# Optimization experiments

Measured on AMD Instinct MI355X. Metric: run time of the kernel, lower is better.

The kernel has to match this reference:

```python
import jax, jax.numpy as jnp
import numpy as np

NUM_HEADS = 8
WINDOW = 33  # must be odd for seq length to be preserved


def setup_inputs() -> dict:
    key = jax.random.key(0)
    ks = jax.random.split(key, 7)
    B, S, E = 4, 2048, 256
    sc = 1.0 / np.sqrt(E)
    return {
        "x": jax.random.normal(ks[0], (B, S, E), dtype=jnp.float32),
        "Wq": jax.random.normal(ks[1], (E, E), dtype=jnp.float32) * sc,
        "bq": jax.random.normal(ks[2], (E,), dtype=jnp.float32) * 0.01,
        "Wk": jax.random.normal(ks[3], (E, E), dtype=jnp.float32) * sc,
        "bk": jax.random.normal(ks[4], (E,), dtype=jnp.float32) * 0.01,
        "Wv": jax.random.normal(ks[5], (E, E), dtype=jnp.float32) * sc,
        "bv": jax.random.normal(ks[6], (E,), dtype=jnp.float32) * 0.01,
    }


def reference(x, Wq, bq, Wk, bk, Wv, bv):
    B, S, E = x.shape
    H = NUM_HEADS
    D = E // H
    W = WINDOW
    pad = (W - 1) // 2
    scale = D ** (-0.5)

    def heads(t):  # [B,S,E] -> [B,H,S,D]
        return t.reshape(B, S, H, D).transpose(0, 2, 1, 3)

    q = heads(x @ Wq + bq)
    k = heads(x @ Wk + bk)
    v = heads(x @ Wv + bv)

    K = S - W + 1  # number of k/v windows (unfold with step=1)
    kv_idx = jnp.arange(K)[:, None] + jnp.arange(W)[None, :]  # [K,W]
    k_unf = k[:, :, kv_idx, :]  # [B,H,K,W,D]
    v_unf = v[:, :, kv_idx, :]  # [B,H,K,W,D]

    q_pad = jnp.pad(q, ((0, 0), (0, 0), (pad, pad), (0, 0)))  # zero pad seq
    q_idx = jnp.arange(S)[:, None] + jnp.arange(W)[None, :]  # [S,W]
    q_unf = q_pad[:, :, q_idx, :]  # [B,H,S,W,D]

    # contract over BOTH window and head dim (faithful to the torch einsums)
    scores = jnp.einsum('bhqwd,bhkwd->bhqk', q_unf, k_unf) * scale  # [B,H,S,K]
    attn = jax.nn.softmax(scores, axis=-1)
    out = jnp.einsum('bhqk,bhkwd->bhqd', attn, v_unf)  # sums v over window too
    return out.transpose(0, 2, 1, 3).reshape(B, S, E)
```

## Files before the change

kernel.cpp:

```cpp
#include <hip/hip_runtime.h>
#include <hip/hip_bf16.h>
#include <math.h>

#define BB   4
#define SS   2048
#define EE   256
#define HH   8
#define DD   32
#define WW   33
#define KKN  (SS - WW + 1)
#define SCALE 0.17677669529663687f
#define FMAX 20.0f
#define SCALE2 0.25503486f
#define FM2    28.853900817779268f

typedef __attribute__((ext_vector_type(8))) short short8v;
typedef __attribute__((ext_vector_type(4))) short short4v;
typedef __attribute__((ext_vector_type(4))) float float4v;

__device__ __forceinline__ short f2bf(float f) {
    union { __hip_bfloat16 h; short s; } c;
    c.h = __float2bfloat16(f);
    return c.s;
}

#if __has_builtin(__builtin_amdgcn_exp2f)
__device__ __forceinline__ float exp2_fast(float x) { return __builtin_amdgcn_exp2f(x); }
#else
__device__ __forceinline__ float exp2_fast(float x) { return __expf(x * 0.6931471805599453f); }
#endif

__global__ __launch_bounds__(256) void qkv_kernel(
    const float* __restrict__ x,
    const float* __restrict__ Wq, const float* __restrict__ bq,
    const float* __restrict__ Wk, const float* __restrict__ bk,
    const float* __restrict__ Wv, const float* __restrict__ bv,
    short* __restrict__ qo, short* __restrict__ ko, float* __restrict__ vo)
{
    __shared__ alignas(16) float xs[64][68];
    __shared__ alignas(16) float ws[64][68];

    const int t   = threadIdx.x;
    const int r0  = blockIdx.x * 64;
    const int ct  = blockIdx.y;
    const int mat = ct >> 2;
    const int cm0 = (ct & 3) * 64;
    const float* Wm   = (mat == 0) ? Wq : (mat == 1) ? Wk : Wv;
    const float* bias = (mat == 0) ? bq : (mat == 1) ? bk : bv;

    const int tr = t >> 4, tc = t & 15;

    float acc[4][4];
#pragma unroll
    for (int i = 0; i < 4; i++)
#pragma unroll
        for (int j = 0; j < 4; j++) acc[i][j] = 0.f;

    for (int ec = 0; ec < 4; ec++) {
        const int e0 = ec * 64;
        __syncthreads();
#pragma unroll
        for (int i = 0; i < 4; i++) {
            int L = t + i * 256;
            int r = L >> 4, c4 = (L & 15) * 4;
            *(float4*)&xs[r][c4] = *(const float4*)(x  + (size_t)(r0 + r) * EE + e0 + c4);
            *(float4*)&ws[r][c4] = *(const float4*)(Wm + (size_t)(e0 + r) * EE + cm0 + c4);
        }
        __syncthreads();

#pragma unroll
        for (int eg = 0; eg < 16; eg++) {
            float4 xv[4], wv4[4];
#pragma unroll
            for (int i = 0; i < 4; i++) xv[i]  = *(const float4*)&xs[tr * 4 + i][eg * 4];
#pragma unroll
            for (int j = 0; j < 4; j++) wv4[j] = *(const float4*)&ws[eg * 4 + j][tc * 4];
            const float* w0p = (const float*)&wv4[0];
            const float* w1p = (const float*)&wv4[1];
            const float* w2p = (const float*)&wv4[2];
            const float* w3p = (const float*)&wv4[3];
#pragma unroll
            for (int i = 0; i < 4; i++)
#pragma unroll
                for (int j = 0; j < 4; j++)
                    acc[i][j] = acc[i][j] + xv[i].x * w0p[j] + xv[i].y * w1p[j]
                                          + xv[i].z * w2p[j] + xv[i].w * w3p[j];
        }
    }

    const int cmb = cm0 + tc * 4;
    const int h = cmb >> 5, d0 = cmb & 31;
    float b4[4];
#pragma unroll
    for (int j = 0; j < 4; j++) b4[j] = bias[cmb + j];

#pragma unroll
    for (int i = 0; i < 4; i++) {
        int row = r0 + tr * 4 + i;
        int b_  = row >> 11;
        int s   = row & 2047;
        size_t o = (((size_t)(b_ * HH + h)) * SS + s) * DD + d0;
        if (mat == 2) {
            float4 vv;
            vv.x = acc[i][0] + b4[0]; vv.y = acc[i][1] + b4[1];
            vv.z = acc[i][2] + b4[2]; vv.w = acc[i][3] + b4[3];
            *(float4*)(vo + o) = vv;
        } else {
            short4v sv;
            sv.x = f2bf(acc[i][0] + b4[0]); sv.y = f2bf(acc[i][1] + b4[1]);
            sv.z = f2bf(acc[i][2] + b4[2]); sv.w = f2bf(acc[i][3] + b4[3]);
            *(short4v*)(((mat == 0) ? qo : ko) + o) = sv;
        }
    }
}

__global__ __launch_bounds__(256) void vs_kernel(
    const float* __restrict__ v, short* __restrict__ vsT)
{
    const int t   = threadIdx.x;
    const int d4  = t & 7;
    const int kkb = blockIdx.x * 32 + (t >> 3);
    const int bh  = blockIdx.y;
    if (kkb >= 252) return;
    const int kb0 = kkb * 8;

    const float4* vp = (const float4*)(v + ((size_t)bh * SS + kb0) * DD) + d4;
    float4 rbuf[7];
    float4 acc = {0.f, 0.f, 0.f, 0.f};
#pragma unroll
    for (int w = 0; w < WW; w++) {
        float4 xv = vp[w * 8];
        if (w < 7) rbuf[w] = xv;
        acc.x += xv.x; acc.y += xv.y; acc.z += xv.z; acc.w += xv.w;
    }
    short8v sh[4];
    sh[0][0] = f2bf(acc.x); sh[1][0] = f2bf(acc.y);
    sh[2][0] = f2bf(acc.z); sh[3][0] = f2bf(acc.w);
#pragma unroll
    for (int s = 1; s < 8; s++) {
        float4 sub = rbuf[s - 1];
        float4 add = vp[(s + 32) * 8];
        acc.x += add.x - sub.x; acc.y += add.y - sub.y;
        acc.z += add.z - sub.z; acc.w += add.w - sub.w;
        sh[0][s] = f2bf(acc.x); sh[1][s] = f2bf(acc.y);
        sh[2][s] = f2bf(acc.z); sh[3][s] = f2bf(acc.w);
    }
#pragma unroll
    for (int j = 0; j < 4; j++) {
        short* op = vsT + ((size_t)bh * DD + 4 * d4 + j) * KKN + kb0;
        *(short8v*)op = sh[j];
    }
}

__global__ __launch_bounds__(256, 4) void attn_kernel(
    const short* __restrict__ qg, const short* __restrict__ kg,
    const short* __restrict__ vsTg, float* __restrict__ out)
{
    __shared__ alignas(16) short QbS[64][40];
    __shared__ alignas(16) short Kb[128][40];
    __shared__ alignas(16) short Gst[96][72];
    __shared__ alignas(16) short vT[2][32][72];
    __shared__ float lrow[32];

    short (*Qb)[40] = QbS;
    short (*pb)[72] = (short (*)[72])QbS;

    const int t  = threadIdx.x;
    const int qt = blockIdx.x;
    const int bh = blockIdx.y;
    const int q0 = qt * 32;

    const short* qb   = qg   + (size_t)bh * SS * DD;
    const short* kb   = kg   + (size_t)bh * SS * DD;
    const short* vsTb = vsTg + (size_t)bh * DD * KKN;

    const int lane = t & 63, wv = t >> 6;
    const int quad = lane >> 4, lr = lane & 15;
    const int ptm = wv >> 1, ptn = wv & 1;
    const int jcol = 64 + (t & 7);

    {
        short8v z = {0, 0, 0, 0, 0, 0, 0, 0};
        short* g = &Gst[0][0];
        for (int i = t; i < 864; i += 256) *(short8v*)(g + 8 * i) = z;
    }

    {
        int row = t >> 2, c8 = (t & 3) * 8;
        int gq = q0 - 16 + row;
        if (gq >= 0 && gq < SS) {
            *(short8v*)&Qb[row][c8] = *(const short8v*)(qb + (size_t)gq * DD + c8);
        } else {
            float4 z = {0.f, 0.f, 0.f, 0.f};
            *(float4*)&Qb[row][c8] = z;
        }
        *(short8v*)&Kb[row][c8]      = *(const short8v*)(kb + (size_t)row * DD + c8);
        *(short8v*)&Kb[64 + row][c8] = *(const short8v*)(kb + (size_t)(64 + row) * DD + c8);
    }
    if (t < 32) lrow[t] = 0.f;
    __syncthreads();

    short8v Qf[4];
#pragma unroll
    for (int tq = 0; tq < 4; tq++)
        Qf[tq] = *(const short8v*)&Qb[tq * 16 + lr][quad * 8];

    short8v Uf[2][2];
#pragma unroll
    for (int qit = 0; qit < 2; qit++)
#pragma unroll
        for (int ch = 0; ch < 2; ch++) {
            short8v u;
#pragma unroll
            for (int j = 0; j < 8; j++) {
                int m  = ch * 32 + quad * 8 + j;
                int qi = qit * 16 + lr;
                u[j] = (qi <= m && m <= qi + 32) ? (short)0x3F80 : (short)0;
            }
            Uf[qit][ch] = u;
        }

    float4v acc = {0.f, 0.f, 0.f, 0.f};
    float lsum[2] = {0.f, 0.f};
    const int npass = (wv < 2) ? 2 : 1;

    for (int kt = 0; kt < 32; kt++) {
        const int k0 = kt * 64;
        {
            int d_ = t >> 3, c8 = (t & 7) * 8;
            int col = k0 + c8; if (col > KKN - 8) col = KKN - 8;
            *(short8v*)&vT[kt & 1][d_][c8] =
                *(const short8v*)(vsTb + (size_t)d_ * KKN + col);
        }

        for (int pass = 0; pass < npass; pass++) {
            const int tk = wv + pass * 4;
            const int gr = k0 + tk * 16 + lr;
            const short8v A = *(const short8v*)&Kb[gr & 127][quad * 8];
#pragma unroll
            for (int tq = 0; tq < 4; tq++) {
                const int del = tk - tq;
                if (del < -2 || del > 4) continue;
                float4v c0 = {0.f, 0.f, 0.f, 0.f};
                c0 = __builtin_amdgcn_mfma_f32_16x16x32_bf16(A, Qf[tq], c0, 0, 0, 0);
                const int i   = tq * 16 + lr;
                const int j2b = tk * 16 + quad * 4 - i + 31;
                short* gbase = &Gst[0][i];
#pragma unroll
                for (int e = 0; e < 4; e++) {
                    int j2 = j2b + e;
                    short* dst = ((unsigned)j2 < 95u) ? (gbase + j2 * 72)
                                                      : (gbase + 95 * 72);
                    *dst = f2bf(c0[e]);
                }
            }
        }

        if (kt > 0) {
            const short8v Ap0 = *(const short8v*)&pb[ptm * 16 + lr][quad * 8];
            const short8v Ap1 = *(const short8v*)&pb[ptm * 16 + lr][32 + quad * 8];
            const short8v Bv0 = *(const short8v*)&vT[(kt - 1) & 1][ptn * 16 + lr][quad * 8];
            const short8v Bv1 = *(const short8v*)&vT[(kt - 1) & 1][ptn * 16 + lr][32 + quad * 8];
            acc = __builtin_amdgcn_mfma_f32_16x16x32_bf16(Ap0, Bv0, acc, 0, 0, 0);
            acc = __builtin_amdgcn_mfma_f32_16x16x32_bf16(Ap1, Bv1, acc, 0, 0, 0);
        }
        __syncthreads();

        if (kt < 31) {
            int r2 = t >> 2, c8 = (t & 3) * 8;
            int g  = k0 + 128 + r2;
            int ga = (g < SS) ? g : (SS - 1);
            *(short8v*)&Kb[g & 127][c8] = *(const short8v*)(kb + (size_t)ga * DD + c8);
        }

        const unsigned lim = (kt == 31) ? 32u : 64u;
        if (kt == 31) {
            short4v z4 = {0, 0, 0, 0};
            int zr = t >> 3, zc = (t & 7) * 4 + 32;
            *(short4v*)&pb[zr][zc] = z4;
        }

        for (int pass = 0; pass < npass; pass++) {
            const int tile = wv + pass * 4;
            const int jrow = tile * 16 + lr;
            const short8v A0f = *(const short8v*)&Gst[jrow][quad * 8];
            const short8v A1f = *(const short8v*)&Gst[jrow][32 + quad * 8];
#pragma unroll
            for (int qit = 0; qit < 2; qit++) {
                float4v D = {0.f, 0.f, 0.f, 0.f};
                D = __builtin_amdgcn_mfma_f32_16x16x32_bf16(A0f, Uf[qit][0], D, 0, 0, 0);
                D = __builtin_amdgcn_mfma_f32_16x16x32_bf16(A1f, Uf[qit][1], D, 0, 0, 0);
                const int qi  = qit * 16 + lr;
                const int kib = qi + tile * 16 + quad * 4 - 31;
                short* prow = &pb[qi][0];
#pragma unroll
                for (int e = 0; e < 4; e++) {
                    int ki = kib + e;
                    float p = exp2_fast(fmaf(D[e], SCALE2, -FM2));
                    bool ok = (unsigned)ki < lim;
                    short* dst = ok ? (prow + ki) : (prow + jcol);
                    *dst = f2bf(p);
                    lsum[qit] += ok ? p : 0.f;
                }
            }
        }
        __syncthreads();
    }

    {
        const short8v Ap0 = *(const short8v*)&pb[ptm * 16 + lr][quad * 8];
        const short8v Ap1 = *(const short8v*)&pb[ptm * 16 + lr][32 + quad * 8];
        const short8v Bv0 = *(const short8v*)&vT[1][ptn * 16 + lr][quad * 8];
        const short8v Bv1 = *(const short8v*)&vT[1][ptn * 16 + lr][32 + quad * 8];
        acc = __builtin_amdgcn_mfma_f32_16x16x32_bf16(Ap0, Bv0, acc, 0, 0, 0);
        acc = __builtin_amdgcn_mfma_f32_16x16x32_bf16(Ap1, Bv1, acc, 0, 0, 0);
    }

#pragma unroll
    for (int qit = 0; qit < 2; qit++) {
        float s = lsum[qit];
        s += __shfl_xor(s, 16);
        s += __shfl_xor(s, 32);
        if (quad == 0) atomicAdd(&lrow[qit * 16 + lr], s);
    }
    __syncthreads();

    {
        const int rrow = ptm * 16 + quad * 4;
        const int col  = ptn * 16 + lr;
        const int b_ = bh >> 3, h = bh & 7;
#pragma unroll
        for (int e = 0; e < 4; e++) {
            int s_ = q0 + rrow + e;
            out[((size_t)(b_ * SS + s_)) * EE + h * DD + col] = acc[e] / lrow[rrow + e];
        }
    }
}

extern "C" void kernel_launch(void* const* d_in, const int* in_sizes, int n_in,
                              void* d_out, int out_size, void* d_ws, size_t ws_size,
                              hipStream_t stream)
{
    (void)in_sizes; (void)n_in; (void)out_size; (void)ws_size;
    const float* x  = (const float*)d_in[0];
    const float* Wq = (const float*)d_in[1];
    const float* bq = (const float*)d_in[2];
    const float* Wk = (const float*)d_in[3];
    const float* bk = (const float*)d_in[4];
    const float* Wv = (const float*)d_in[5];
    const float* bv = (const float*)d_in[6];
    float* out = (float*)d_out;

    const size_t REG = (size_t)BB * HH * SS * DD;
    short* qbf   = (short*)d_ws;
    short* kbf   = qbf + REG;
    float* vbuf  = (float*)(kbf + REG);
    short* vsTb  = (short*)(vbuf + REG);

    qkv_kernel<<<dim3(128, 12), dim3(256), 0, stream>>>(x, Wq, bq, Wk, bk, Wv, bv,
                                                        qbf, kbf, vbuf);
    vs_kernel<<<dim3(8, 32), dim3(256), 0, stream>>>(vbuf, vsTb);
    attn_kernel<<<dim3(64, 32), dim3(256), 0, stream>>>(qbf, kbf, vsTb, out);
}
```

Baseline: 301.8 us.

## Rebalance softmax tile work across waves, pack bf16 conversions, add MFMA priority hints

The softmax/probability stage now assigns each wave a single query sub-tile and three key tiles, instead of having two waves do two passes over both query sub-tiles, so the work is spread evenly over all four waves. Float-to-bf16 conversions are paired with a packed two-element conversion, and s_setprio is raised around MFMA groups. Separately, vs_kernel is relaunched with 64-thread blocks over more blocks. Risks include extra scheduling constraints from the priority hints and a small shift in occupancy.

```diff
diff --git a/kernel.cpp b/kernel.cpp
--- a/kernel.cpp
+++ b/kernel.cpp
@@ -21,6 +21,13 @@
 __device__ __forceinline__ short f2bf(float f) {
     union { __hip_bfloat16 h; short s; } c;
     c.h = __float2bfloat16(f);
+    return c.s;
+}
+
+__device__ __forceinline__ short2 f2bf2(float a, float b) {
+    union { __hip_bfloat162 h; short2 s; } c;
+    float2 f; f.x = a; f.y = b;
+    c.h = __float22bfloat162_rn(f);
     return c.s;
 }
 
@@ -114,12 +121,12 @@
     }
 }
 
-__global__ __launch_bounds__(256) void vs_kernel(
+__global__ __launch_bounds__(64) void vs_kernel(
     const float* __restrict__ v, short* __restrict__ vsT)
 {
     const int t   = threadIdx.x;
     const int d4  = t & 7;
-    const int kkb = blockIdx.x * 32 + (t >> 3);
+    const int kkb = blockIdx.x * 8 + (t >> 3);
     const int bh  = blockIdx.y;
     if (kkb >= 252) return;
     const int kb0 = kkb * 8;
@@ -179,6 +186,10 @@
     const int ptm = wv >> 1, ptn = wv & 1;
     const int jcol = 64 + (t & 7);
 
+    const int qitw  = wv & 1;
+    const int tbase = wv >> 1;
+    const int qi    = qitw * 16 + lr;
+
     {
         short8v z = {0, 0, 0, 0, 0, 0, 0, 0};
         short* g = &Gst[0][0];
@@ -205,23 +216,20 @@
     for (int tq = 0; tq < 4; tq++)
         Qf[tq] = *(const short8v*)&Qb[tq * 16 + lr][quad * 8];
 
-    short8v Uf[2][2];
-#pragma unroll
-    for (int qit = 0; qit < 2; qit++)
-#pragma unroll
-        for (int ch = 0; ch < 2; ch++) {
-            short8v u;
-#pragma unroll
-            for (int j = 0; j < 8; j++) {
-                int m  = ch * 32 + quad * 8 + j;
-                int qi = qit * 16 + lr;
-                u[j] = (qi <= m && m <= qi + 32) ? (short)0x3F80 : (short)0;
-            }
-            Uf[qit][ch] = u;
-        }
+    short8v Ufw[2];
+#pragma unroll
+    for (int ch = 0; ch < 2; ch++) {
+        short8v u;
+#pragma unroll
+        for (int j = 0; j < 8; j++) {
+            int m = ch * 32 + quad * 8 + j;
+            u[j] = (qi <= m && m <= qi + 32) ? (short)0x3F80 : (short)0;
+        }
+        Ufw[ch] = u;
+    }
 
     float4v acc = {0.f, 0.f, 0.f, 0.f};
-    float lsum[2] = {0.f, 0.f};
+    float lsumw = 0.f;
     const int npass = (wv < 2) ? 2 : 1;
 
     for (int kt = 0; kt < 32; kt++) {
@@ -246,12 +254,15 @@
                 const int i   = tq * 16 + lr;
                 const int j2b = tk * 16 + quad * 4 - i + 31;
                 short* gbase = &Gst[0][i];
+                short2 g01 = f2bf2(c0[0], c0[1]);
+                short2 g23 = f2bf2(c0[2], c0[3]);
+                short gv[4] = {g01.x, g01.y, g23.x, g23.y};
 #pragma unroll
                 for (int e = 0; e < 4; e++) {
                     int j2 = j2b + e;
                     short* dst = ((unsigned)j2 < 95u) ? (gbase + j2 * 72)
                                                       : (gbase + 95 * 72);
-                    *dst = f2bf(c0[e]);
+                    *dst = gv[e];
                 }
             }
         }
@@ -261,8 +272,10 @@
             const short8v Ap1 = *(const short8v*)&pb[ptm * 16 + lr][32 + quad * 8];
             const short8v Bv0 = *(const short8v*)&vT[(kt - 1) & 1][ptn * 16 + lr][quad * 8];
             const short8v Bv1 = *(const short8v*)&vT[(kt - 1) & 1][ptn * 16 + lr][32 + quad * 8];
+            __builtin_amdgcn_s_setprio(1);
             acc = __builtin_amdgcn_mfma_f32_16x16x32_bf16(Ap0, Bv0, acc, 0, 0, 0);
             acc = __builtin_amdgcn_mfma_f32_16x16x32_bf16(Ap1, Bv1, acc, 0, 0, 0);
+            __builtin_amdgcn_s_setprio(0);
         }
         __syncthreads();
 
@@ -280,28 +293,34 @@
             *(short4v*)&pb[zr][zc] = z4;
         }
 
-        for (int pass = 0; pass < npass; pass++) {
-            const int tile = wv + pass * 4;
+        short* prow = &pb[qi][0];
+#pragma unroll
+        for (int u = 0; u < 3; u++) {
+            const int tile = 2 * u + tbase;
             const int jrow = tile * 16 + lr;
             const short8v A0f = *(const short8v*)&Gst[jrow][quad * 8];
             const short8v A1f = *(const short8v*)&Gst[jrow][32 + quad * 8];
-#pragma unroll
-            for (int qit = 0; qit < 2; qit++) {
-                float4v D = {0.f, 0.f, 0.f, 0.f};
-                D = __builtin_amdgcn_mfma_f32_16x16x32_bf16(A0f, Uf[qit][0], D, 0, 0, 0);
-                D = __builtin_amdgcn_mfma_f32_16x16x32_bf16(A1f, Uf[qit][1], D, 0, 0, 0);
-                const int qi  = qit * 16 + lr;
-                const int kib = qi + tile * 16 + quad * 4 - 31;
-                short* prow = &pb[qi][0];
-#pragma unroll
-                for (int e = 0; e < 4; e++) {
-                    int ki = kib + e;
-                    float p = exp2_fast(fmaf(D[e], SCALE2, -FM2));
-                    bool ok = (unsigned)ki < lim;
-                    short* dst = ok ? (prow + ki) : (prow + jcol);
-                    *dst = f2bf(p);
-                    lsum[qit] += ok ? p : 0.f;
-                }
+            float4v D = {0.f, 0.f, 0.f, 0.f};
+            __builtin_amdgcn_s_setprio(1);
+            D = __builtin_amdgcn_mfma_f32_16x16x32_bf16(A0f, Ufw[0], D, 0, 0, 0);
+            D = __builtin_amdgcn_mfma_f32_16x16x32_bf16(A1f, Ufw[1], D, 0, 0, 0);
+            __builtin_amdgcn_s_setprio(0);
+            const int kib = qi + tile * 16 + quad * 4 - 31;
+            float p0 = exp2_fast(fmaf(D[0], SCALE2, -FM2));
+            float p1 = exp2_fast(fmaf(D[1], SCALE2, -FM2));
+            float p2 = exp2_fast(fmaf(D[2], SCALE2, -FM2));
+            float p3 = exp2_fast(fmaf(D[3], SCALE2, -FM2));
+            short2 c01 = f2bf2(p0, p1);
+            short2 c23 = f2bf2(p2, p3);
+            float pv[4] = {p0, p1, p2, p3};
+            short cv[4] = {c01.x, c01.y, c23.x, c23.y};
+#pragma unroll
+            for (int e = 0; e < 4; e++) {
+                int ki = kib + e;
+                bool ok = (unsigned)ki < lim;
+                short* dst = ok ? (prow + ki) : (prow + jcol);
+                *dst = cv[e];
+                lsumw += ok ? pv[e] : 0.f;
             }
         }
         __syncthreads();
@@ -316,12 +335,11 @@
         acc = __builtin_amdgcn_mfma_f32_16x16x32_bf16(Ap1, Bv1, acc, 0, 0, 0);
     }
 
-#pragma unroll
-    for (int qit = 0; qit < 2; qit++) {
-        float s = lsum[qit];
+    {
+        float s = lsumw;
         s += __shfl_xor(s, 16);
         s += __shfl_xor(s, 32);
-        if (quad == 0) atomicAdd(&lrow[qit * 16 + lr], s);
+        if (quad == 0) atomicAdd(&lrow[qitw * 16 + lr], s);
     }
     __syncthreads();
 
@@ -359,6 +377,6 @@
 
     qkv_kernel<<<dim3(128, 12), dim3(256), 0, stream>>>(x, Wq, bq, Wk, bk, Wv, bv,
                                                         qbf, kbf, vbuf);
-    vs_kernel<<<dim3(8, 32), dim3(256), 0, stream>>>(vbuf, vsTb);
+    vs_kernel<<<dim3(32, 32), dim3(64), 0, stream>>>(vbuf, vsTb);
     attn_kernel<<<dim3(64, 32), dim3(256), 0, stream>>>(qbf, kbf, vsTb, out);
 }
```

New measurement: 271.5 us. 10.0% less time.
